# Performance work log

Measured on AMD Instinct MI355X. Metric: run time of the kernel, lower is better.

Reference implementation:

```python
import jax, jax.numpy as jnp
import numpy as np
from jax import lax

B, S, D, H, T = 128, 512, 128, 128, 20


def setup_inputs() -> dict:
    key = jax.random.key(0)
    ks = jax.random.split(key, 16)
    sc = 1.0 / np.sqrt(H)
    u = lambda k, shape: jax.random.uniform(k, shape, jnp.float32, -sc, sc)
    return {
        "inputs": jax.random.normal(ks[0], (B, S, D), jnp.float32),
        "tags": jax.random.randint(ks[1], (B, S), 0, T),
        "mask": jnp.ones((B, S), jnp.bool_),
        "w_ih_f": u(ks[2], (4 * H, D)),
        "w_hh_f": u(ks[3], (4 * H, H)),
        "b_f": u(ks[4], (4 * H,)),
        "w_ih_b": u(ks[5], (4 * H, D)),
        "w_hh_b": u(ks[6], (4 * H, H)),
        "b_b": u(ks[7], (4 * H,)),
        "w_out": u(ks[8], (T, 2 * H)),
        "b_out": u(ks[9], (T,)),
        "start_trans": jax.random.uniform(ks[10], (T,), jnp.float32, -0.1, 0.1),
        "end_trans": jax.random.uniform(ks[11], (T,), jnp.float32, -0.1, 0.1),
        "trans": jax.random.uniform(ks[12], (T, T), jnp.float32, -0.1, 0.1),
    }


def _lstm_dir(x, w_ih, w_hh, b, reverse):
    # x: [B,S,D] -> hidden states [B,S,H]
    xp = jnp.einsum('bsd,gd->bsg', x, w_ih) + b  # precomputed input gates [B,S,4H]
    if reverse:
        xp = xp[:, ::-1]
    h0 = jnp.zeros((x.shape[0], H), x.dtype)
    c0 = jnp.zeros((x.shape[0], H), x.dtype)

    def step(carry, xt):
        h, c = carry
        g = xt + h @ w_hh.T
        i, f, gg, o = jnp.split(g, 4, axis=-1)
        i, f, o = jax.nn.sigmoid(i), jax.nn.sigmoid(f), jax.nn.sigmoid(o)
        c = f * c + i * jnp.tanh(gg)
        h = o * jnp.tanh(c)
        return (h, c), h

    _, hs = lax.scan(step, (h0, c0), xp.transpose(1, 0, 2))
    hs = hs.transpose(1, 0, 2)  # [B,S,H]
    if reverse:
        hs = hs[:, ::-1]
    return hs


def _crf_nll(em, tags, mask, start_trans, end_trans, trans):
    # em: [B,S,T]; torchcrf log-likelihood, reduction='mean', negated
    b, s, t = em.shape
    maskf = mask.astype(em.dtype)
    batch = jnp.arange(b)
    # numerator: score of the gold path
    num = start_trans[tags[:, 0]] + em[batch, 0, tags[:, 0]]
    em_tag = jnp.take_along_axis(em, tags[:, :, None], axis=2)[:, :, 0]  # [B,S]
    trans_tag = trans[tags[:, :-1], tags[:, 1:]]  # [B,S-1]
    num = num + jnp.sum((trans_tag + em_tag[:, 1:]) * maskf[:, 1:], axis=1)
    seq_ends = jnp.sum(mask.astype(jnp.int32), axis=1) - 1
    num = num + end_trans[tags[batch, seq_ends]]
    # denominator: forward algorithm (logsumexp semiring) via scan
    score0 = start_trans[None, :] + em[:, 0]  # [B,T]

    def step(score, inp):
        em_t, m_t = inp
        nxt = jax.nn.logsumexp(score[:, :, None] + trans[None] + em_t[:, None, :], axis=1)
        return jnp.where(m_t[:, None], nxt, score), None

    score, _ = lax.scan(step, score0, (em[:, 1:].transpose(1, 0, 2), mask[:, 1:].T))
    den = jax.nn.logsumexp(score + end_trans[None, :], axis=1)
    return -jnp.mean(num - den)


def reference(inputs, tags, mask, w_ih_f, w_hh_f, b_f, w_ih_b, w_hh_b, b_b,
              w_out, b_out, start_trans, end_trans, trans):
    h_f = _lstm_dir(inputs, w_ih_f, w_hh_f, b_f, reverse=False)
    h_b = _lstm_dir(inputs, w_ih_b, w_hh_b, b_b, reverse=True)
    lstm_out = jnp.concatenate([h_f, h_b], axis=-1)  # [B,S,2H]
    emissions = jnp.einsum('bsh,th->bst', lstm_out, w_out) + b_out  # [B,S,T]
    return _crf_nll(emissions, tags, mask, start_trans, end_trans, trans)
```

## Files before the change

kernel.cpp:

```cpp
#include <hip/hip_runtime.h>
#include <cstdint>
#include <cstddef>

#define DEVINL __device__ __forceinline__

constexpr int Bz = 128, Sl = 512, Dm = 128, Hd = 128, NC = 1024, Tt = 20;
constexpr int Mrows = Bz * Sl;

constexpr size_t OFF_XP   = 17043456;
constexpr size_t OFF_HS   = 151261184;
constexpr size_t OFF_EM   = 184815616;
constexpr size_t OFF_PART = 190058496;

DEVINL unsigned short f2bf(float f) {
    uint32_t u = __float_as_uint(f);
    u += 0x7fffu + ((u >> 16) & 1u);
    return (unsigned short)(u >> 16);
}
DEVINL float bf2f(unsigned short h) { return __uint_as_float(((uint32_t)h) << 16); }

DEVINL float rcpf(float x) { return __builtin_amdgcn_rcpf(x); }

DEVINL void barrier_lds_only() {
    __asm__ __volatile__("s_waitcnt lgkmcnt(0)" ::: "memory");
    __builtin_amdgcn_s_barrier();
    __asm__ __volatile__("" ::: "memory");
}

template <int CTRL>
DEVINL float qperm(float v) {
    int i = __float_as_int(v);
    int r = __builtin_amdgcn_update_dpp(i, i, CTRL, 0xF, 0xF, true);
    return __int_as_float(r);
}

typedef __attribute__((ext_vector_type(8))) __bf16 bf16x8;
typedef __attribute__((ext_vector_type(4))) float f32x4;
typedef _Float16 __attribute__((ext_vector_type(2))) half2_t;
typedef _Float16 __attribute__((ext_vector_type(8))) half8_t;

__global__ __launch_bounds__(256, 2) void gemm_xp_k(
    const float* __restrict__ X, const float* __restrict__ wihf, const float* __restrict__ wihb,
    const float* __restrict__ b_f, const float* __restrict__ b_b,
    unsigned short* __restrict__ xp)
{
    __shared__ __align__(16) unsigned short As[64 * 132];
    __shared__ __align__(16) unsigned short Bs[128 * 132];
    const int m0 = blockIdx.x * 64;
    const int tid = threadIdx.x;
    const int wave = tid >> 6, lane = tid & 63;
    const int wm = (wave >> 1) * 32, wn = (wave & 1) * 64;
    const int ln = lane & 15, qd = lane >> 4;
    const int colc = (tid & 31) * 4, rowb = tid >> 5;

    #pragma unroll
    for (int r = 0; r < 8; ++r) {
        int row = rowb + r * 8;
        float4 av = *(const float4*)(&X[(size_t)(m0 + row) * 128 + colc]);
        ushort4 au; au.x = f2bf(av.x); au.y = f2bf(av.y); au.z = f2bf(av.z); au.w = f2bf(av.w);
        *(ushort4*)(&As[row * 132 + colc]) = au;
    }

    const int bidx = m0 >> 9;
    const int tbase = m0 & 511;

    for (int nt = 0; nt < 8; ++nt) {
        const float* Bsrc = (nt < 4) ? (wihf + (size_t)nt * 128 * 128)
                                     : (wihb + (size_t)(nt - 4) * 128 * 128);
        __syncthreads();
        #pragma unroll
        for (int r = 0; r < 16; ++r) {
            int row = rowb + r * 8;
            float4 bv = *(const float4*)(&Bsrc[(size_t)row * 128 + colc]);
            ushort4 bu; bu.x = f2bf(bv.x); bu.y = f2bf(bv.y); bu.z = f2bf(bv.z); bu.w = f2bf(bv.w);
            *(ushort4*)(&Bs[row * 132 + colc]) = bu;
        }
        __syncthreads();

        f32x4 acc[2][4] = {};
        #pragma unroll
        for (int kk = 0; kk < 4; ++kk) {
            const int kb = kk * 32 + qd * 8;
            bf16x8 af[2], bfr[4];
            #pragma unroll
            for (int i = 0; i < 2; ++i)
                af[i] = *(const bf16x8*)(&As[(wm + i * 16 + ln) * 132 + kb]);
            #pragma unroll
            for (int j = 0; j < 4; ++j)
                bfr[j] = *(const bf16x8*)(&Bs[(wn + j * 16 + ln) * 132 + kb]);
            #pragma unroll
            for (int i = 0; i < 2; ++i)
                #pragma unroll
                for (int j = 0; j < 4; ++j)
                    acc[i][j] = __builtin_amdgcn_mfma_f32_16x16x32_bf16(af[i], bfr[j], acc[i][j], 0, 0, 0);
        }
        #pragma unroll
        for (int j = 0; j < 4; ++j) {
            const int col = nt * 128 + wn + j * 16 + ln;
            const float bv = (col < 512) ? b_f[col] : b_b[col - 512];
            #pragma unroll
            for (int i = 0; i < 2; ++i) {
                const int tloc = tbase + wm + i * 16 + qd * 4;
                ushort4 o;
                o.x = f2bf(acc[i][j][0] + bv); o.y = f2bf(acc[i][j][1] + bv);
                o.z = f2bf(acc[i][j][2] + bv); o.w = f2bf(acc[i][j][3] + bv);
                *(ushort4*)(xp + ((size_t)bidx * 1024 + col) * 512 + tloc) = o;
            }
        }
    }
}

__global__ __launch_bounds__(512, 1) void lstm_k(
    const float* __restrict__ whf, const float* __restrict__ whb,
    const unsigned short* __restrict__ xp, unsigned short* __restrict__ hs)
{
    __shared__ __align__(16) _Float16 h_buf[2][128];
    const int dir = blockIdx.x >> 7;
    const int b   = blockIdx.x & 127;
    const int tid = threadIdx.x;
    const int lane = tid & 63;
    const int wv   = tid >> 6;
    const int q    = lane & 3;
    const int u    = wv * 16 + (lane >> 2);
    const int grow = q * 128 + u;

    const float* wsrc = dir ? whb : whf;
    half2_t w2[4][16];
    #pragma unroll
    for (int g = 0; g < 4; ++g) {
        const float* wrow = wsrc + (size_t)(g * 128 + u) * 128 + q * 32;
        #pragma unroll
        for (int k = 0; k < 16; ++k)
            w2[g][k] = half2_t{(_Float16)wrow[2 * k], (_Float16)wrow[2 * k + 1]};
    }

    const float S  = (q == 2) ? 2.f : 1.f;
    const float Aa = (q == 2) ? 2.f : 1.f;
    const float Bc = (q == 2) ? -1.f : 0.f;

    if (tid < 128) { h_buf[0][tid] = (_Float16)0.f; h_buf[1][tid] = (_Float16)0.f; }
    __syncthreads();

    const unsigned short* xrow = xp + ((size_t)b * 1024 + dir * 512 + grow) * 512;
    unsigned short* hptr = hs + (size_t)dir * Mrows * 128 + (size_t)b * Sl * 128 + u
                              + (dir ? (size_t)(Sl - 1) * 128 : 0);
    const int hstep = dir ? -128 : 128;

    float c = 0.f;
    ushort4 cur;
    {
        ushort4 r = *(const ushort4*)(xrow + (dir ? 508 : 0));
        cur = dir ? ushort4{r.w, r.z, r.y, r.x} : r;
    }

    for (int t = 0; t < Sl; t += 4) {
        const int tn = (t + 4 < Sl) ? (t + 4) : 0;
        ushort4 nraw = *(const ushort4*)(xrow + (dir ? (508 - tn) : tn));

        #pragma unroll
        for (int s = 0; s < 4; ++s) {
            const int p = s & 1;
            const unsigned short xb = (s == 0) ? cur.x : (s == 1) ? cur.y : (s == 2) ? cur.z : cur.w;
            float xv = bf2f(xb);

            const half8_t* hp = (const half8_t*)&h_buf[p][q * 32];
            float p0 = 0.f, p1 = 0.f, p2 = 0.f, p3 = 0.f;
            #pragma unroll
            for (int k = 0; k < 4; ++k) {
                half8_t hv = hp[k];
                const half2_t* h2 = (const half2_t*)&hv;
                #pragma unroll
                for (int j = 0; j < 4; ++j) {
                    p0 = __builtin_amdgcn_fdot2(w2[0][4 * k + j], h2[j], p0, false);
                    p1 = __builtin_amdgcn_fdot2(w2[1][4 * k + j], h2[j], p1, false);
                    p2 = __builtin_amdgcn_fdot2(w2[2][4 * k + j], h2[j], p2, false);
                    p3 = __builtin_amdgcn_fdot2(w2[3][4 * k + j], h2[j], p3, false);
                }
            }
            float keep0 = (q & 1) ? p1 : p0;
            float send0 = (q & 1) ? p0 : p1;
            float keep1 = (q & 1) ? p3 : p2;
            float send1 = (q & 1) ? p2 : p3;
            float s0 = keep0 + qperm<0xB1>(send0);
            float s1 = keep1 + qperm<0xB1>(send1);
            float keep2 = (q & 2) ? s1 : s0;
            float send2 = (q & 2) ? s0 : s1;
            float tot = keep2 + qperm<0x4E>(send2) + xv;

            float act = Aa * rcpf(1.f + __expf(-S * tot)) + Bc;
            float a0 = qperm<0x00>(act);
            float a1 = qperm<0x55>(act);
            float a2 = qperm<0xAA>(act);
            float a3 = qperm<0xFF>(act);
            c = fmaf(a1, c, a0 * a2);
            float th = 1.f - 2.f * rcpf(1.f + __expf(2.f * c));
            float h = a3 * th;
            if (q == 0) {
                _Float16 hh = (_Float16)h;
                h_buf[1 - p][u] = hh;
                unsigned short hbits; __builtin_memcpy(&hbits, &hh, 2);
                *hptr = hbits;
            }
            hptr += hstep;
            barrier_lds_only();
        }
        cur = dir ? ushort4{nraw.w, nraw.z, nraw.y, nraw.x} : nraw;
    }
}

__global__ __launch_bounds__(320, 1) void emis_k(
    const unsigned short* __restrict__ hs, const float* __restrict__ wout,
    const float* __restrict__ bout, float* __restrict__ em)
{
    __shared__ __align__(16) half2_t wlds[20 * 128];
    const int b  = blockIdx.x >> 2;
    const int qt = blockIdx.x & 3;
    const int tid = threadIdx.x;

    #pragma unroll
    for (int k = 0; k < 8; ++k) {
        int i = tid + k * 320;
        wlds[i] = half2_t{(_Float16)wout[2 * i], (_Float16)wout[2 * i + 1]};
    }
    __syncthreads();

    const int tag  = tid % 20;
    const int copy = tid / 20;
    half2_t wreg[128];
    {
        const uint4* wl4 = (const uint4*)&wlds[tag * 128];
        #pragma unroll
        for (int k = 0; k < 32; ++k) {
            uint4 v = wl4[k];
            __builtin_memcpy(&wreg[4 * k], &v, 16);
        }
    }
    const float bo = bout[tag];
    const unsigned short* hf_base = hs + (size_t)b * Sl * 128;
    const unsigned short* hb_base = hs + (size_t)Mrows * 128 + (size_t)b * Sl * 128;

    #pragma unroll
    for (int i = 0; i < 8; ++i) {
        const int t = qt * 128 + copy + 16 * i;
        const uint4* hf4 = (const uint4*)(hf_base + (size_t)t * 128);
        const uint4* hb4 = (const uint4*)(hb_base + (size_t)t * 128);
        float a0 = bo, a1 = 0.f, a2 = 0.f, a3 = 0.f;
        #pragma unroll
        for (int k = 0; k < 16; ++k) {
            uint4 v = hf4[k];
            half2_t h2[4]; __builtin_memcpy(h2, &v, 16);
            a0 = __builtin_amdgcn_fdot2(wreg[4 * k + 0], h2[0], a0, false);
            a1 = __builtin_amdgcn_fdot2(wreg[4 * k + 1], h2[1], a1, false);
            a2 = __builtin_amdgcn_fdot2(wreg[4 * k + 2], h2[2], a2, false);
            a3 = __builtin_amdgcn_fdot2(wreg[4 * k + 3], h2[3], a3, false);
        }
        #pragma unroll
        for (int k = 0; k < 16; ++k) {
            uint4 v = hb4[k];
            half2_t h2[4]; __builtin_memcpy(h2, &v, 16);
            a0 = __builtin_amdgcn_fdot2(wreg[64 + 4 * k + 0], h2[0], a0, false);
            a1 = __builtin_amdgcn_fdot2(wreg[64 + 4 * k + 1], h2[1], a1, false);
            a2 = __builtin_amdgcn_fdot2(wreg[64 + 4 * k + 2], h2[2], a2, false);
            a3 = __builtin_amdgcn_fdot2(wreg[64 + 4 * k + 3], h2[3], a3, false);
        }
        em[((size_t)b * Sl + t) * Tt + tag] = (a0 + a1) + (a2 + a3);
    }
}

__global__ __launch_bounds__(64) void crf_k(
    const float* __restrict__ em, const int* __restrict__ tags,
    const float* __restrict__ st, const float* __restrict__ et,
    const float* __restrict__ trans, float* __restrict__ part)
{
    const int b = blockIdx.x, lane = threadIdx.x;
    const float* emb = em + (size_t)b * Sl * Tt;
    const int* tg = tags + (size_t)b * Sl;

    float nacc = 0.f;
    for (int t = 1 + lane; t < Sl; t += 64) {
        int tp = tg[t - 1], tc = tg[t];
        nacc += trans[tp * Tt + tc] + emb[t * Tt + tc];
    }
    #pragma unroll
    for (int off = 32; off; off >>= 1) nacc += __shfl_down(nacc, off);

    float Etr[20];
    #pragma unroll
    for (int i = 0; i < 20; ++i)
        Etr[i] = (lane < 20) ? __expf(trans[i * Tt + lane]) : 0.f;

    float C = 0.f;
    float p = (lane < 20) ? __expf(st[lane] + emb[lane]) : 0.f;

    float evr[8];
    #pragma unroll
    for (int s = 0; s < 8; ++s) {
        int tt = 1 + s; tt = tt < Sl ? tt : Sl - 1;
        evr[s] = (lane < 20) ? emb[(size_t)tt * Tt + lane] : 0.f;
    }

    for (int t0 = 1; t0 < Sl; t0 += 8) {
        #pragma unroll
        for (int s = 0; s < 8; ++s) {
            const int t = t0 + s;
            if (t < Sl) {
                float ev = evr[s];
                int tf = t + 8; tf = tf < Sl ? tf : Sl - 1;
                evr[s] = (lane < 20) ? emb[(size_t)tf * Tt + lane] : 0.f;

                float q0 = 0.f, q1 = 0.f, q2 = 0.f, q3 = 0.f;
                #pragma unroll
                for (int i = 0; i < 20; i += 4) {
                    q0 = fmaf(__int_as_float(__builtin_amdgcn_readlane(__float_as_int(p), i + 0)), Etr[i + 0], q0);
                    q1 = fmaf(__int_as_float(__builtin_amdgcn_readlane(__float_as_int(p), i + 1)), Etr[i + 1], q1);
                    q2 = fmaf(__int_as_float(__builtin_amdgcn_readlane(__float_as_int(p), i + 2)), Etr[i + 2], q2);
                    q3 = fmaf(__int_as_float(__builtin_amdgcn_readlane(__float_as_int(p), i + 3)), Etr[i + 3], q3);
                }
                p = ((q0 + q1) + (q2 + q3)) * __expf(ev);
                if ((s & 3) == 3) {
                    float S0 = 0.f, S1 = 0.f, S2 = 0.f, S3 = 0.f;
                    #pragma unroll
                    for (int i = 0; i < 20; i += 4) {
                        S0 += __int_as_float(__builtin_amdgcn_readlane(__float_as_int(p), i + 0));
                        S1 += __int_as_float(__builtin_amdgcn_readlane(__float_as_int(p), i + 1));
                        S2 += __int_as_float(__builtin_amdgcn_readlane(__float_as_int(p), i + 2));
                        S3 += __int_as_float(__builtin_amdgcn_readlane(__float_as_int(p), i + 3));
                    }
                    float Ssum = (S0 + S1) + (S2 + S3);
                    C += __logf(Ssum);
                    p *= rcpf(Ssum);
                }
            }
        }
    }
    float f = (lane < 20) ? p * __expf(et[lane]) : 0.f;
    float S0 = 0.f, S1 = 0.f, S2 = 0.f, S3 = 0.f;
    #pragma unroll
    for (int i = 0; i < 20; i += 4) {
        S0 += __int_as_float(__builtin_amdgcn_readlane(__float_as_int(f), i + 0));
        S1 += __int_as_float(__builtin_amdgcn_readlane(__float_as_int(f), i + 1));
        S2 += __int_as_float(__builtin_amdgcn_readlane(__float_as_int(f), i + 2));
        S3 += __int_as_float(__builtin_amdgcn_readlane(__float_as_int(f), i + 3));
    }
    float den = C + __logf((S0 + S1) + (S2 + S3));
    if (lane == 0)
        part[b] = nacc + st[tg[0]] + emb[tg[0]] + et[tg[Sl - 1]] - den;
}

__global__ void fin_k(const float* __restrict__ part, float* __restrict__ out) {
    int l = threadIdx.x;
    float v = part[l] + part[l + 64];
    #pragma unroll
    for (int off = 32; off; off >>= 1) v += __shfl_xor(v, off);
    if (l == 0) out[0] = -v * (1.f / 128.f);
}

extern "C" void kernel_launch(void* const* d_in, const int* in_sizes, int n_in,
                              void* d_out, int out_size, void* d_ws, size_t ws_size,
                              hipStream_t stream) {
    const float* x      = (const float*)d_in[0];
    const int*   tags   = (const int*)d_in[1];
    const float* w_ih_f = (const float*)d_in[3];
    const float* w_hh_f = (const float*)d_in[4];
    const float* b_f    = (const float*)d_in[5];
    const float* w_ih_b = (const float*)d_in[6];
    const float* w_hh_b = (const float*)d_in[7];
    const float* b_b    = (const float*)d_in[8];
    const float* w_out  = (const float*)d_in[9];
    const float* b_out  = (const float*)d_in[10];
    const float* st     = (const float*)d_in[11];
    const float* et     = (const float*)d_in[12];
    const float* trans  = (const float*)d_in[13];
    float* out = (float*)d_out;

    char* ws = (char*)d_ws;
    unsigned short* xp   = (unsigned short*)(ws + OFF_XP);
    unsigned short* hs   = (unsigned short*)(ws + OFF_HS);
    float*          em   = (float*)(ws + OFF_EM);
    float*          part = (float*)(ws + OFF_PART);

    gemm_xp_k<<<Mrows / 64, 256, 0, stream>>>(x, w_ih_f, w_ih_b, b_f, b_b, xp);
    lstm_k<<<256, 512, 0, stream>>>(w_hh_f, w_hh_b, xp, hs);
    emis_k<<<Bz * 4, 320, 0, stream>>>(hs, w_out, b_out, em);
    crf_k<<<Bz, 64, 0, stream>>>(em, tags, st, et, trans, part);
    fin_k<<<1, 64, 0, stream>>>(part, out);
}
```

Baseline: 524.7 us.

## Compute LSTM recurrent matvec with MFMA 16x16x32 f16 instead of fdot2

```diff
diff --git a/kernel.cpp b/kernel.cpp
--- a/kernel.cpp
+++ b/kernel.cpp
@@ -25,13 +25,6 @@
     __asm__ __volatile__("s_waitcnt lgkmcnt(0)" ::: "memory");
     __builtin_amdgcn_s_barrier();
     __asm__ __volatile__("" ::: "memory");
-}
-
-template <int CTRL>
-DEVINL float qperm(float v) {
-    int i = __float_as_int(v);
-    int r = __builtin_amdgcn_update_dpp(i, i, CTRL, 0xF, 0xF, true);
-    return __int_as_float(r);
 }
 
 typedef __attribute__((ext_vector_type(8))) __bf16 bf16x8;
@@ -114,97 +107,109 @@
     const float* __restrict__ whf, const float* __restrict__ whb,
     const unsigned short* __restrict__ xp, unsigned short* __restrict__ hs)
 {
-    __shared__ __align__(16) _Float16 h_buf[2][128];
+    __shared__ __align__(16) _Float16 h_lds[2][136];
     const int dir = blockIdx.x >> 7;
     const int b   = blockIdx.x & 127;
     const int tid = threadIdx.x;
+    const int w    = tid >> 6;
     const int lane = tid & 63;
-    const int wv   = tid >> 6;
-    const int q    = lane & 3;
-    const int u    = wv * 16 + (lane >> 2);
-    const int grow = q * 128 + u;
-
-    const float* wsrc = dir ? whb : whf;
-    half2_t w2[4][16];
-    #pragma unroll
-    for (int g = 0; g < 4; ++g) {
-        const float* wrow = wsrc + (size_t)(g * 128 + u) * 128 + q * 32;
-        #pragma unroll
-        for (int k = 0; k < 16; ++k)
-            w2[g][k] = half2_t{(_Float16)wrow[2 * k], (_Float16)wrow[2 * k + 1]};
-    }
-
-    const float S  = (q == 2) ? 2.f : 1.f;
-    const float Aa = (q == 2) ? 2.f : 1.f;
-    const float Bc = (q == 2) ? -1.f : 0.f;
-
-    if (tid < 128) { h_buf[0][tid] = (_Float16)0.f; h_buf[1][tid] = (_Float16)0.f; }
+    const int ln = lane & 15, q = lane >> 4;
+    const int r  = ln & 3;
+    const int u  = w * 16 + q * 4 + r;
+
+    const float* W = dir ? whb : whf;
+    half8_t af[4][4];
+    #pragma unroll
+    for (int g = 0; g < 4; ++g)
+        #pragma unroll
+        for (int kc = 0; kc < 4; ++kc) {
+            const float* src = W + (size_t)(g * 128 + w * 16 + ln) * 128 + kc * 32 + q * 8;
+            #pragma unroll
+            for (int j = 0; j < 8; ++j) af[g][kc][j] = (_Float16)src[j];
+        }
+
+    if (tid < 136) { h_lds[0][tid] = (_Float16)0.f; h_lds[1][tid] = (_Float16)0.f; }
     __syncthreads();
 
-    const unsigned short* xrow = xp + ((size_t)b * 1024 + dir * 512 + grow) * 512;
-    unsigned short* hptr = hs + (size_t)dir * Mrows * 128 + (size_t)b * Sl * 128 + u
+    const unsigned short* xbase = xp + ((size_t)b * 1024 + dir * 512 + w * 16 + q * 4) * 512;
+    unsigned short* hout = hs + (size_t)dir * Mrows * 128 + (size_t)b * Sl * 128 + u
                               + (dir ? (size_t)(Sl - 1) * 128 : 0);
     const int hstep = dir ? -128 : 128;
 
     float c = 0.f;
-    ushort4 cur;
+    ushort4 xb[4][4];
     {
-        ushort4 r = *(const ushort4*)(xrow + (dir ? 508 : 0));
-        cur = dir ? ushort4{r.w, r.z, r.y, r.x} : r;
+        const int tl = dir ? 508 : 0;
+        #pragma unroll
+        for (int g = 0; g < 4; ++g)
+            #pragma unroll
+            for (int rr = 0; rr < 4; ++rr) {
+                ushort4 v = *(const ushort4*)(xbase + (size_t)(g * 128 + rr) * 512 + tl);
+                xb[g][rr] = dir ? ushort4{v.w, v.z, v.y, v.x} : v;
+            }
     }
 
     for (int t = 0; t < Sl; t += 4) {
         const int tn = (t + 4 < Sl) ? (t + 4) : 0;
-        ushort4 nraw = *(const ushort4*)(xrow + (dir ? (508 - tn) : tn));
+        const int tl = dir ? (508 - tn) : tn;
+        ushort4 xn[4][4];
+        #pragma unroll
+        for (int g = 0; g < 4; ++g)
+            #pragma unroll
+            for (int rr = 0; rr < 4; ++rr) {
+                ushort4 v = *(const ushort4*)(xbase + (size_t)(g * 128 + rr) * 512 + tl);
+                xn[g][rr] = dir ? ushort4{v.w, v.z, v.y, v.x} : v;
+            }
 
         #pragma unroll
         for (int s = 0; s < 4; ++s) {
-            const int p = s & 1;
-            const unsigned short xb = (s == 0) ? cur.x : (s == 1) ? cur.y : (s == 2) ? cur.z : cur.w;
-            float xv = bf2f(xb);
-
-            const half8_t* hp = (const half8_t*)&h_buf[p][q * 32];
-            float p0 = 0.f, p1 = 0.f, p2 = 0.f, p3 = 0.f;
-            #pragma unroll
-            for (int k = 0; k < 4; ++k) {
-                half8_t hv = hp[k];
-                const half2_t* h2 = (const half2_t*)&hv;
+            const int p = (t + s) & 1;
+            f32x4 acc[4];
+            #pragma unroll
+            for (int g = 0; g < 4; ++g) {
                 #pragma unroll
-                for (int j = 0; j < 4; ++j) {
-                    p0 = __builtin_amdgcn_fdot2(w2[0][4 * k + j], h2[j], p0, false);
-                    p1 = __builtin_amdgcn_fdot2(w2[1][4 * k + j], h2[j], p1, false);
-                    p2 = __builtin_amdgcn_fdot2(w2[2][4 * k + j], h2[j], p2, false);
-                    p3 = __builtin_amdgcn_fdot2(w2[3][4 * k + j], h2[j], p3, false);
+                for (int rr = 0; rr < 4; ++rr) {
+                    const ushort4 v = xb[g][rr];
+                    const unsigned short x16 = (s == 0) ? v.x : (s == 1) ? v.y : (s == 2) ? v.z : v.w;
+                    acc[g][rr] = bf2f(x16);
                 }
             }
-            float keep0 = (q & 1) ? p1 : p0;
-            float send0 = (q & 1) ? p0 : p1;
-            float keep1 = (q & 1) ? p3 : p2;
-            float send1 = (q & 1) ? p2 : p3;
-            float s0 = keep0 + qperm<0xB1>(send0);
-            float s1 = keep1 + qperm<0xB1>(send1);
-            float keep2 = (q & 2) ? s1 : s0;
-            float send2 = (q & 2) ? s0 : s1;
-            float tot = keep2 + qperm<0x4E>(send2) + xv;
-
-            float act = Aa * rcpf(1.f + __expf(-S * tot)) + Bc;
-            float a0 = qperm<0x00>(act);
-            float a1 = qperm<0x55>(act);
-            float a2 = qperm<0xAA>(act);
-            float a3 = qperm<0xFF>(act);
-            c = fmaf(a1, c, a0 * a2);
-            float th = 1.f - 2.f * rcpf(1.f + __expf(2.f * c));
-            float h = a3 * th;
-            if (q == 0) {
+            half8_t bfr[4];
+            #pragma unroll
+            for (int kc = 0; kc < 4; ++kc)
+                bfr[kc] = *(const half8_t*)(&h_lds[p][kc * 32 + q * 8]);
+            #pragma unroll
+            for (int g = 0; g < 4; ++g)
+                #pragma unroll
+                for (int kc = 0; kc < 4; ++kc)
+                    acc[g] = __builtin_amdgcn_mfma_f32_16x16x32_f16(af[g][kc], bfr[kc], acc[g], 0, 0, 0);
+
+            float v[4];
+            #pragma unroll
+            for (int g = 0; g < 4; ++g) {
+                float x0 = (r & 1) ? acc[g][1] : acc[g][0];
+                float x1 = (r & 1) ? acc[g][3] : acc[g][2];
+                v[g] = (r & 2) ? x1 : x0;
+            }
+            float gi = rcpf(1.f + __expf(-v[0]));
+            float gf = rcpf(1.f + __expf(-v[1]));
+            float gg = 1.f - 2.f * rcpf(1.f + __expf(2.f * v[2]));
+            float go = rcpf(1.f + __expf(-v[3]));
+            c = fmaf(gf, c, gi * gg);
+            float h = go * (1.f - 2.f * rcpf(1.f + __expf(2.f * c)));
+            if (ln < 4) {
                 _Float16 hh = (_Float16)h;
-                h_buf[1 - p][u] = hh;
+                h_lds[1 - p][u] = hh;
                 unsigned short hbits; __builtin_memcpy(&hbits, &hh, 2);
-                *hptr = hbits;
-            }
-            hptr += hstep;
+                *hout = hbits;
+            }
+            hout += hstep;
             barrier_lds_only();
         }
-        cur = dir ? ushort4{nraw.w, nraw.z, nraw.y, nraw.x} : nraw;
+        #pragma unroll
+        for (int g = 0; g < 4; ++g)
+            #pragma unroll
+            for (int rr = 0; rr < 4; ++rr) xb[g][rr] = xn[g][rr];
     }
 }
 
```

After: 673.3 us. +28.3%, slower.
